# Performance work log

Measured on AMD Instinct MI355X. Metric: run time of the kernel, lower is better.

The kernel has to match this reference:

```python
import jax, jax.numpy as jnp
import numpy as np

HIDDEN = 512
LATENT = 256
BATCH = 1024
SEQ_LEN = 256


def setup_inputs() -> dict:
    key = jax.random.key(0)
    ks = jax.random.split(key, 12)
    s_h = 1.0 / np.sqrt(2 * HIDDEN)
    s_c = 1.0 / np.sqrt(LATENT)
    return {
        "h": jax.random.normal(ks[0], (BATCH, HIDDEN), jnp.float32),
        "c": jax.random.normal(ks[1], (BATCH, HIDDEN), jnp.float32),
        "seq_len": SEQ_LEN,
        # init-state projections: Linear(2*hidden, latent)
        "init_h_W": jax.random.uniform(ks[2], (LATENT, 2 * HIDDEN), jnp.float32, -s_h, s_h),
        "init_h_b": jax.random.uniform(ks[3], (LATENT,), jnp.float32, -s_h, s_h),
        "init_c_W": jax.random.uniform(ks[4], (LATENT, 2 * HIDDEN), jnp.float32, -s_h, s_h),
        "init_c_b": jax.random.uniform(ks[5], (LATENT,), jnp.float32, -s_h, s_h),
        # LSTM cell: input dim = hidden, state dim = latent, gates stacked [i, f, g, o]
        "W_ih": jax.random.uniform(ks[6], (4 * LATENT, HIDDEN), jnp.float32, -s_c, s_c),
        "W_hh": jax.random.uniform(ks[7], (4 * LATENT, LATENT), jnp.float32, -s_c, s_c),
        "b_ih": jax.random.uniform(ks[8], (4 * LATENT,), jnp.float32, -s_c, s_c),
        "b_hh": jax.random.uniform(ks[9], (4 * LATENT,), jnp.float32, -s_c, s_c),
    }


def reference(h, c, seq_len, init_h_W, init_h_b, init_c_W, init_c_b, W_ih, W_hh, b_ih, b_hh):
    # init states: ELU(Linear(cat(h, c)))
    hc = jnp.concatenate([h, c], axis=1)                     # [B, 2H]
    h_t = jax.nn.elu(hc @ init_h_W.T + init_h_b)             # [B, L]
    c_t = jax.nn.elu(hc @ init_c_W.T + init_c_b)             # [B, L]

    # input to the cell is the constant encoder state h -> precompute its projection once
    x_proj = h @ W_ih.T + b_ih + b_hh                        # [B, 4L]

    def step(carry, _):
        h_t, c_t = carry
        gates = x_proj + h_t @ W_hh.T                        # [B, 4L]
        i, f, g, o = jnp.split(gates, 4, axis=1)
        c_n = jax.nn.sigmoid(f) * c_t + jax.nn.sigmoid(i) * jnp.tanh(g)
        h_n = jax.nn.sigmoid(o) * jnp.tanh(c_n)
        return (h_n, c_n), h_n

    _, ys = jax.lax.scan(step, (h_t, c_t), None, length=seq_len)  # ys: [T, B, L]
    return jnp.transpose(ys, (1, 0, 2))                      # [B, T, L]
```

## Files before the change

kernel.cpp:

```cpp
#include <hip/hip_runtime.h>
#include <stdint.h>

typedef __attribute__((ext_vector_type(4))) float f32x4;
typedef __attribute__((ext_vector_type(8))) _Float16 f16x8;

static __device__ __forceinline__ unsigned short f2h(float f) {
    union { _Float16 h; unsigned short u; } v;
    v.h = (_Float16)f;
    return v.u;
}
static __device__ __forceinline__ float h2f_lo(unsigned int u) {
    union { unsigned short s; _Float16 h; } v; v.s = (unsigned short)(u & 0xffffu);
    return (float)v.h;
}
static __device__ __forceinline__ float h2f_hi(unsigned int u) {
    union { unsigned short s; _Float16 h; } v; v.s = (unsigned short)(u >> 16);
    return (float)v.h;
}
static __device__ __forceinline__ f16x8 as_f16x8(uint4 v) {
    union { uint4 u; f16x8 s; } x; x.u = v; return x.s;
}
static __device__ __forceinline__ float sigmoid_fast(float x) {
    return __builtin_amdgcn_rcpf(1.0f + __builtin_amdgcn_exp2f(-1.4426950408889634f * x));
}
static __device__ __forceinline__ float tanh_fast(float x) {
    return 1.0f - 2.0f * __builtin_amdgcn_rcpf(1.0f + __builtin_amdgcn_exp2f(2.8853900817779268f * x));
}
static __device__ __forceinline__ void lds_barrier() {
    __builtin_amdgcn_s_waitcnt(0xc07f);
    __builtin_amdgcn_s_barrier();
}

__global__ __launch_bounds__(256) void convert_all(
    const float* __restrict__ h, const float* __restrict__ c,
    const float* __restrict__ iWh, const float* __restrict__ iWc,
    const float* __restrict__ Wih, const float* __restrict__ Whh,
    unsigned short* __restrict__ hc_h, unsigned short* __restrict__ iWh_h,
    unsigned short* __restrict__ iWc_h, unsigned short* __restrict__ Wih_h,
    unsigned short* __restrict__ Whh_h) {
    int i = blockIdx.x * 256 + threadIdx.x;
    const float* src; unsigned short* dst;
    if (i < 131072) {
        int base = i * 4, r = base >> 9, cc = base & 511;
        src = h + base; dst = hc_h + r * 1024 + cc;
    } else if (i < 262144) {
        int j = i - 131072; int base = j * 4, r = base >> 9, cc = base & 511;
        src = c + base; dst = hc_h + r * 1024 + 512 + cc;
    } else if (i < 327680) { int j = i - 262144; src = iWh + j * 4; dst = iWh_h + j * 4; }
    else if (i < 393216)   { int j = i - 327680; src = iWc + j * 4; dst = iWc_h + j * 4; }
    else if (i < 524288)   { int j = i - 393216; src = Wih + j * 4; dst = Wih_h + j * 4; }
    else                   { int j = i - 524288; src = Whh + j * 4; dst = Whh_h + j * 4; }
    float4 v = *(const float4*)src;
    dst[0] = f2h(v.x); dst[1] = f2h(v.y); dst[2] = f2h(v.z); dst[3] = f2h(v.w);
}

__global__ __launch_bounds__(256) void gemm_bt(
    const unsigned short* __restrict__ A, const unsigned short* __restrict__ W,
    float* __restrict__ C, const float* __restrict__ b1, const float* __restrict__ b2,
    int K, int lda, int ldw, int N, int do_elu, int bias_row) {
    __shared__ unsigned short As[64][40];
    __shared__ unsigned short Bs[64][40];
    int tid = threadIdx.x;
    int lane = tid & 63, wv = tid >> 6;
    int q = lane >> 4, l15 = lane & 15;
    int Mbase = blockIdx.x * 64, Nbase = blockIdx.y * 64;
    int ldrow = tid >> 2, seg = tid & 3;
    const unsigned short* Ap = A + (size_t)(Mbase + ldrow) * lda + seg * 8;
    const unsigned short* Wp = W + (size_t)(Nbase + ldrow) * ldw + seg * 8;
    f32x4 acc[4] = {};
    for (int k0 = 0; k0 < K; k0 += 32) {
        uint4 av = *(const uint4*)(Ap + k0);
        uint4 wvv = *(const uint4*)(Wp + k0);
        __syncthreads();
        *(uint4*)(&As[ldrow][seg * 8]) = av;
        *(uint4*)(&Bs[ldrow][seg * 8]) = wvv;
        __syncthreads();
        f16x8 af = *(const f16x8*)(&As[wv * 16 + l15][q * 8]);
#pragma unroll
        for (int nt = 0; nt < 4; nt++) {
            f16x8 bf = *(const f16x8*)(&Bs[nt * 16 + l15][q * 8]);
            acc[nt] = __builtin_amdgcn_mfma_f32_16x16x32_f16(af, bf, acc[nt], 0, 0, 0);
        }
    }
#pragma unroll
    for (int nt = 0; nt < 4; nt++) {
        int col = Nbase + nt * 16 + l15;
        float bcol = bias_row ? 0.0f : (b1[col] + (b2 ? b2[col] : 0.0f));
#pragma unroll
        for (int r = 0; r < 4; r++) {
            int row = Mbase + wv * 16 + q * 4 + r;
            float bias = bias_row ? (b1[row] + (b2 ? b2[row] : 0.0f)) : bcol;
            float v = acc[nt][r] + bias;
            if (do_elu) v = v > 0.0f ? v : (__builtin_amdgcn_exp2f(1.4426950408889634f * v) - 1.0f);
            C[(size_t)row * N + col] = v;
        }
    }
}

__global__ __launch_bounds__(256) void gemm_init(
    const unsigned short* __restrict__ A,
    const unsigned short* __restrict__ W0, const unsigned short* __restrict__ W1,
    float* __restrict__ C0, float* __restrict__ C1,
    const float* __restrict__ bias0, const float* __restrict__ bias1) {
    const unsigned short* W = blockIdx.z ? W1 : W0;
    float* C = blockIdx.z ? C1 : C0;
    const float* bias = blockIdx.z ? bias1 : bias0;
    __shared__ unsigned short As[64][40];
    __shared__ unsigned short Bs[64][40];
    int tid = threadIdx.x;
    int lane = tid & 63, wv = tid >> 6;
    int q = lane >> 4, l15 = lane & 15;
    int Mbase = blockIdx.x * 64, Nbase = blockIdx.y * 64;
    int ldrow = tid >> 2, seg = tid & 3;
    const unsigned short* Ap = A + (size_t)(Mbase + ldrow) * 1024 + seg * 8;
    const unsigned short* Wp = W + (size_t)(Nbase + ldrow) * 1024 + seg * 8;
    f32x4 acc[4] = {};
    for (int k0 = 0; k0 < 1024; k0 += 32) {
        uint4 av = *(const uint4*)(Ap + k0);
        uint4 wvv = *(const uint4*)(Wp + k0);
        __syncthreads();
        *(uint4*)(&As[ldrow][seg * 8]) = av;
        *(uint4*)(&Bs[ldrow][seg * 8]) = wvv;
        __syncthreads();
        f16x8 af = *(const f16x8*)(&As[wv * 16 + l15][q * 8]);
#pragma unroll
        for (int nt = 0; nt < 4; nt++) {
            f16x8 bf = *(const f16x8*)(&Bs[nt * 16 + l15][q * 8]);
            acc[nt] = __builtin_amdgcn_mfma_f32_16x16x32_f16(af, bf, acc[nt], 0, 0, 0);
        }
    }
#pragma unroll
    for (int nt = 0; nt < 4; nt++) {
        int col = Nbase + nt * 16 + l15;
        float b = bias[col];
#pragma unroll
        for (int r = 0; r < 4; r++) {
            int row = Mbase + wv * 16 + q * 4 + r;
            float v = acc[nt][r] + b;
            v = v > 0.0f ? v : (__builtin_amdgcn_exp2f(1.4426950408889634f * v) - 1.0f);
            C[(size_t)row * 256 + col] = v;
        }
    }
}

#define HB_STRIDE 264
#define HB_HALF   (16 * HB_STRIDE)
#define WLDS_OFF  (2 * HB_HALF * 2)
#define WFRAGS    17
#define LSTM_LDS_BYTES (WLDS_OFF + 8 * WFRAGS * 1024)

__global__ __launch_bounds__(512, 2) void lstm_rec(
    const unsigned short* __restrict__ Whh,
    const float* __restrict__ xpT,
    const float* __restrict__ h0,
    const float* __restrict__ c0,
    const int* __restrict__ seq_len,
    float* __restrict__ out)
{
    __shared__ uint4 smem4[LSTM_LDS_BYTES / 16];
    unsigned short* hbuf = (unsigned short*)smem4;
    unsigned char* wlds = (unsigned char*)smem4 + WLDS_OFF;
    const int tid = threadIdx.x;
    const int lane = tid & 63, wv = tid >> 6;
    const int q = lane >> 4, l15 = lane & 15;
    const int T = *seq_len;
    const int rowbase = blockIdx.x * 16;

    {
        int e = tid * 8;
        int r = e >> 8, cc = e & 255;
        const float* s = h0 + (size_t)(rowbase + r) * 256 + cc;
        float4 v0 = *(const float4*)s;
        float4 v1 = *(const float4*)(s + 4);
        unsigned short* d = hbuf + r * HB_STRIDE + cc;
        d[0] = f2h(v0.x); d[1] = f2h(v0.y); d[2] = f2h(v0.z); d[3] = f2h(v0.w);
        d[4] = f2h(v1.x); d[5] = f2h(v1.y); d[6] = f2h(v1.z); d[7] = f2h(v1.w);
    }

    const unsigned short* wb = Whh + wv * 8192 + l15 * 256 + q * 8;

    uint4 wreg[47];
#pragma unroll
    for (int kt = 0; kt < 6; kt++)
#pragma unroll
        for (int g = 0; g < 4; g++)
#pragma unroll
            for (int ct = 0; ct < 2; ct++) {
                int fi = kt * 8 + g * 2 + ct;
                if (fi < 47)
                    wreg[fi] = *(const uint4*)(wb + (size_t)g * 65536 + ct * 4096 + kt * 32);
            }

    unsigned char* wlp = wlds + wv * (WFRAGS * 1024) + lane * 16;
#pragma unroll
    for (int fi = 0; fi < WFRAGS; fi++) {
        int kt = (fi < 8) ? 6 : (fi < 16 ? 7 : 5);
        int p  = (fi < 16) ? (fi & 7) : 7;
        int g = p >> 1, ct = p & 1;
        uint4 v = *(const uint4*)(wb + (size_t)g * 65536 + ct * 4096 + kt * 32);
        *(uint4*)(wlp + fi * 1024) = v;
    }

    float creg[8];
#pragma unroll
    for (int ct = 0; ct < 2; ct++)
#pragma unroll
        for (int r = 0; r < 4; r++)
            creg[ct * 4 + r] = c0[(size_t)(rowbase + q * 4 + r) * 256 + wv * 32 + ct * 16 + l15];

    unsigned int xph[16];
    {
        const float* xpb = xpT + (size_t)(wv * 32 + l15) * 1024 + rowbase + (q << 2);
#pragma unroll
        for (int p = 0; p < 8; p++) {
            f32x4 v = *(const f32x4*)(xpb + (size_t)(p >> 1) * 262144 + (p & 1) * 16384);
            xph[p * 2]     = (unsigned int)f2h(v[0]) | ((unsigned int)f2h(v[1]) << 16);
            xph[p * 2 + 1] = (unsigned int)f2h(v[2]) | ((unsigned int)f2h(v[3]) << 16);
        }
    }

    float* outp = out + ((size_t)(rowbase + q * 4) * T) * 256 + wv * 32 + l15;

    __syncthreads();

    for (int t = 0; t < T; t++) {
        const unsigned short* hb = hbuf + (t & 1) * HB_HALF + l15 * HB_STRIDE + q * 8;
        f32x4 acc[8];
#pragma unroll
        for (int p = 0; p < 8; p++) {
            acc[p][0] = 0.0f; acc[p][1] = 0.0f; acc[p][2] = 0.0f; acc[p][3] = 0.0f;
        }
#pragma unroll
        for (int kt = 0; kt < 8; kt++) {
            f16x8 af = *(const f16x8*)(hb + kt * 32);
#pragma unroll
            for (int p = 0; p < 8; p++) {
                f16x8 bf;
                if (kt < 6 && !(kt == 5 && p == 7))
                    bf = as_f16x8(wreg[kt * 8 + p]);
                else if (kt == 6)
                    bf = *(const f16x8*)(wlp + p * 1024);
                else if (kt == 7)
                    bf = *(const f16x8*)(wlp + (8 + p) * 1024);
                else
                    bf = *(const f16x8*)(wlp + 16 * 1024);
                acc[p] = __builtin_amdgcn_mfma_f32_16x16x32_f16(af, bf, acc[p], 0, 0, 0);
            }
        }
        float hv[8];
#pragma unroll
        for (int ct = 0; ct < 2; ct++)
#pragma unroll
            for (int r = 0; r < 4; r++) {
                int w = r >> 1;
                float xi = (r & 1) ? h2f_hi(xph[(0 + ct) * 2 + w]) : h2f_lo(xph[(0 + ct) * 2 + w]);
                float xf = (r & 1) ? h2f_hi(xph[(2 + ct) * 2 + w]) : h2f_lo(xph[(2 + ct) * 2 + w]);
                float xg = (r & 1) ? h2f_hi(xph[(4 + ct) * 2 + w]) : h2f_lo(xph[(4 + ct) * 2 + w]);
                float xo = (r & 1) ? h2f_hi(xph[(6 + ct) * 2 + w]) : h2f_lo(xph[(6 + ct) * 2 + w]);
                float ig = sigmoid_fast(acc[0 + ct][r] + xi);
                float fg = sigmoid_fast(acc[2 + ct][r] + xf);
                float gg = tanh_fast(acc[4 + ct][r] + xg);
                float og = sigmoid_fast(acc[6 + ct][r] + xo);
                float cn = fg * creg[ct * 4 + r] + ig * gg;
                creg[ct * 4 + r] = cn;
                hv[ct * 4 + r] = og * tanh_fast(cn);
            }
        unsigned short* hn = hbuf + ((t + 1) & 1) * HB_HALF + (q * 4) * HB_STRIDE + wv * 32 + l15;
#pragma unroll
        for (int ct = 0; ct < 2; ct++)
#pragma unroll
            for (int r = 0; r < 4; r++)
                hn[r * HB_STRIDE + ct * 16] = f2h(hv[ct * 4 + r]);
#pragma unroll
        for (int ct = 0; ct < 2; ct++)
#pragma unroll
            for (int r = 0; r < 4; r++)
                outp[(size_t)r * T * 256 + ct * 16] = hv[ct * 4 + r];
        outp += 256;
        lds_barrier();
    }
}

extern "C" void kernel_launch(void* const* d_in, const int* in_sizes, int n_in,
                              void* d_out, int out_size, void* d_ws, size_t ws_size,
                              hipStream_t stream) {
    const float* h   = (const float*)d_in[0];
    const float* c   = (const float*)d_in[1];
    const int*   seqp= (const int*)d_in[2];
    const float* iWh = (const float*)d_in[3];
    const float* ibh = (const float*)d_in[4];
    const float* iWc = (const float*)d_in[5];
    const float* ibc = (const float*)d_in[6];
    const float* Wih = (const float*)d_in[7];
    const float* Whh = (const float*)d_in[8];
    const float* bih = (const float*)d_in[9];
    const float* bhh = (const float*)d_in[10];
    float* out = (float*)d_out;
    unsigned char* ws = (unsigned char*)d_ws;

    unsigned short* hc_h  = (unsigned short*)(ws + 0);
    unsigned short* iWh_h = (unsigned short*)(ws + 2097152);
    unsigned short* iWc_h = (unsigned short*)(ws + 2621440);
    unsigned short* Wih_h = (unsigned short*)(ws + 3145728);
    unsigned short* Whh_h = (unsigned short*)(ws + 4194304);
    float* h0  = (float*)(ws + 4718592);
    float* c0  = (float*)(ws + 5767168);
    float* xpT = (float*)(ws + 6815744);

    convert_all<<<2304, 256, 0, stream>>>(h, c, iWh, iWc, Wih, Whh,
                                          hc_h, iWh_h, iWc_h, Wih_h, Whh_h);

    gemm_init<<<dim3(16, 4, 2), 256, 0, stream>>>(hc_h, iWh_h, iWc_h, h0, c0, ibh, ibc);
    gemm_bt<<<dim3(16, 16), 256, 0, stream>>>(Wih_h, hc_h, xpT, bih, bhh,
                                              512, 512, 1024, 1024, 0, 1);

    lstm_rec<<<64, 512, 0, stream>>>(Whh_h, xpT, h0, c0, seqp, out);
}
```

Before: 1.302 ms.

## Split recurrent MFMA into two passes and interleave ct=0 gate math

The per-step recurrent GEMM is split into two passes. The first computes the even-indexed accumulators (the ct=0 column tile of every gate) at raised wave priority. The second computes the odd-indexed accumulators and interleaves the elementwise LSTM update, LDS h store and global output store for ct=0 between its MFMAs, so transcendental and store work overlaps matrix-core work. The LDS h pointer is duplicated through an empty asm to stop the compiler merging the two passes' loads. This raises register pressure and relies on the compiler keeping the intended schedule.

```diff
diff --git a/kernel.cpp b/kernel.cpp
--- a/kernel.cpp
+++ b/kernel.cpp
@@ -223,62 +223,79 @@
 
     __syncthreads();
 
+#define EW_STORE(ct, r) do { \
+        const int w_ = (r) >> 1; \
+        float xi = ((r) & 1) ? h2f_hi(xph[(0 + (ct)) * 2 + w_]) : h2f_lo(xph[(0 + (ct)) * 2 + w_]); \
+        float xf = ((r) & 1) ? h2f_hi(xph[(2 + (ct)) * 2 + w_]) : h2f_lo(xph[(2 + (ct)) * 2 + w_]); \
+        float xg = ((r) & 1) ? h2f_hi(xph[(4 + (ct)) * 2 + w_]) : h2f_lo(xph[(4 + (ct)) * 2 + w_]); \
+        float xo = ((r) & 1) ? h2f_hi(xph[(6 + (ct)) * 2 + w_]) : h2f_lo(xph[(6 + (ct)) * 2 + w_]); \
+        float ig = sigmoid_fast(acc[0 + (ct)][(r)] + xi); \
+        float fg = sigmoid_fast(acc[2 + (ct)][(r)] + xf); \
+        float gg = tanh_fast(acc[4 + (ct)][(r)] + xg); \
+        float og = sigmoid_fast(acc[6 + (ct)][(r)] + xo); \
+        float cn = fg * creg[(ct) * 4 + (r)] + ig * gg; \
+        creg[(ct) * 4 + (r)] = cn; \
+        float hv = og * tanh_fast(cn); \
+        hn[(r) * HB_STRIDE + (ct) * 16] = f2h(hv); \
+        outp[(size_t)(r) * T * 256 + (ct) * 16] = hv; \
+    } while (0)
+
     for (int t = 0; t < T; t++) {
         const unsigned short* hb = hbuf + (t & 1) * HB_HALF + l15 * HB_STRIDE + q * 8;
+        unsigned short* hn = hbuf + ((t + 1) & 1) * HB_HALF + (q * 4) * HB_STRIDE + wv * 32 + l15;
+        const unsigned short* hb2 = hb;
+        asm("" : "+v"(hb2));
+
         f32x4 acc[8];
 #pragma unroll
         for (int p = 0; p < 8; p++) {
             acc[p][0] = 0.0f; acc[p][1] = 0.0f; acc[p][2] = 0.0f; acc[p][3] = 0.0f;
         }
+
+        __builtin_amdgcn_s_setprio(1);
 #pragma unroll
         for (int kt = 0; kt < 8; kt++) {
             f16x8 af = *(const f16x8*)(hb + kt * 32);
 #pragma unroll
-            for (int p = 0; p < 8; p++) {
+            for (int g = 0; g < 4; g++) {
+                const int p = g * 2;
                 f16x8 bf;
-                if (kt < 6 && !(kt == 5 && p == 7))
-                    bf = as_f16x8(wreg[kt * 8 + p]);
-                else if (kt == 6)
-                    bf = *(const f16x8*)(wlp + p * 1024);
-                else if (kt == 7)
-                    bf = *(const f16x8*)(wlp + (8 + p) * 1024);
-                else
-                    bf = *(const f16x8*)(wlp + 16 * 1024);
+                if (kt < 6)       bf = as_f16x8(wreg[kt * 8 + p]);
+                else if (kt == 6) bf = *(const f16x8*)(wlp + p * 1024);
+                else              bf = *(const f16x8*)(wlp + (8 + p) * 1024);
                 acc[p] = __builtin_amdgcn_mfma_f32_16x16x32_f16(af, bf, acc[p], 0, 0, 0);
             }
         }
-        float hv[8];
-#pragma unroll
-        for (int ct = 0; ct < 2; ct++)
-#pragma unroll
-            for (int r = 0; r < 4; r++) {
-                int w = r >> 1;
-                float xi = (r & 1) ? h2f_hi(xph[(0 + ct) * 2 + w]) : h2f_lo(xph[(0 + ct) * 2 + w]);
-                float xf = (r & 1) ? h2f_hi(xph[(2 + ct) * 2 + w]) : h2f_lo(xph[(2 + ct) * 2 + w]);
-                float xg = (r & 1) ? h2f_hi(xph[(4 + ct) * 2 + w]) : h2f_lo(xph[(4 + ct) * 2 + w]);
-                float xo = (r & 1) ? h2f_hi(xph[(6 + ct) * 2 + w]) : h2f_lo(xph[(6 + ct) * 2 + w]);
-                float ig = sigmoid_fast(acc[0 + ct][r] + xi);
-                float fg = sigmoid_fast(acc[2 + ct][r] + xf);
-                float gg = tanh_fast(acc[4 + ct][r] + xg);
-                float og = sigmoid_fast(acc[6 + ct][r] + xo);
-                float cn = fg * creg[ct * 4 + r] + ig * gg;
-                creg[ct * 4 + r] = cn;
-                hv[ct * 4 + r] = og * tanh_fast(cn);
+        __builtin_amdgcn_s_setprio(0);
+
+#pragma unroll
+        for (int kt = 0; kt < 8; kt++) {
+            f16x8 af = *(const f16x8*)(hb2 + kt * 32);
+#pragma unroll
+            for (int g = 0; g < 4; g++) {
+                const int p = g * 2 + 1;
+                f16x8 bf;
+                if (kt < 6 && !(kt == 5 && p == 7)) bf = as_f16x8(wreg[kt * 8 + p]);
+                else if (kt == 6) bf = *(const f16x8*)(wlp + p * 1024);
+                else if (kt == 7) bf = *(const f16x8*)(wlp + (8 + p) * 1024);
+                else              bf = *(const f16x8*)(wlp + 16 * 1024);
+                acc[p] = __builtin_amdgcn_mfma_f32_16x16x32_f16(af, bf, acc[p], 0, 0, 0);
             }
-        unsigned short* hn = hbuf + ((t + 1) & 1) * HB_HALF + (q * 4) * HB_STRIDE + wv * 32 + l15;
-#pragma unroll
-        for (int ct = 0; ct < 2; ct++)
-#pragma unroll
-            for (int r = 0; r < 4; r++)
-                hn[r * HB_STRIDE + ct * 16] = f2h(hv[ct * 4 + r]);
-#pragma unroll
-        for (int ct = 0; ct < 2; ct++)
-#pragma unroll
-            for (int r = 0; r < 4; r++)
-                outp[(size_t)r * T * 256 + ct * 16] = hv[ct * 4 + r];
+            if (kt == 1) EW_STORE(0, 0);
+            if (kt == 3) EW_STORE(0, 1);
+            if (kt == 5) EW_STORE(0, 2);
+            if (kt == 7) EW_STORE(0, 3);
+        }
+
+        EW_STORE(1, 0);
+        EW_STORE(1, 1);
+        EW_STORE(1, 2);
+        EW_STORE(1, 3);
+
         outp += 256;
         lds_barrier();
     }
+#undef EW_STORE
 }
 
 extern "C" void kernel_launch(void* const* d_in, const int* in_sizes, int n_in,
```

Result: slower. 1.745 ms (+34.1%).
